# Kernel tuning notes

Measured on AMD Instinct MI355X. Metric: run time of the kernel, lower is better.

The kernel has to match this reference:

```python
import jax, jax.numpy as jnp
import numpy as np

N_NODES = 1_000_000
N_EDGES = 4_000_000  # knn_k = 4
N_GRAPHS = 1024
HIDDEN = 64
N_FEAT = 4


def setup_inputs() -> dict:
    key = jax.random.key(0)
    k0, k1, k2, k3, k4 = jax.random.split(key, 5)
    x = jax.random.normal(k0, (N_NODES, N_FEAT), dtype=jnp.float32)
    edge_index = jax.random.randint(k1, (2, N_EDGES), 0, N_NODES, dtype=jnp.int64)
    batch = jnp.sort(jax.random.randint(k2, (N_NODES,), 0, N_GRAPHS, dtype=jnp.int64))
    W1 = jax.random.normal(k3, (N_FEAT, HIDDEN), dtype=jnp.float32) * 0.5
    b1 = jnp.zeros((HIDDEN,), dtype=jnp.float32)
    W2 = jax.random.normal(k4, (HIDDEN, 1), dtype=jnp.float32) * 0.1
    b2 = jnp.zeros((1,), dtype=jnp.float32)
    return {"x": x, "W1": W1, "b1": b1, "W2": W2, "b2": b2,
            "edge_index": edge_index, "batch": batch}


def gcn_conv(x, edge_index, W, b):
    # PyG GCNConv: linear transform, add self-loops, sym-normalize, scatter-add.
    n = x.shape[0]
    h = x @ W  # [N, 64]
    loop = jnp.arange(n, dtype=edge_index.dtype)
    row = jnp.concatenate([edge_index[0], loop])  # source j
    col = jnp.concatenate([edge_index[1], loop])  # target i
    deg = jax.ops.segment_sum(jnp.ones_like(col, dtype=h.dtype), col, num_segments=n)
    dis = jnp.where(deg > 0, jax.lax.rsqrt(jnp.maximum(deg, 1.0)), 0.0)
    norm = dis[row] * dis[col]  # [E+N]
    out = jax.ops.segment_sum(h[row] * norm[:, None], col, num_segments=n)
    return out + b


def reference(x, W1, b1, W2, b2, edge_index, batch):
    h = gcn_conv(x, edge_index, W1, b1)          # [N, 64]
    h = jax.nn.elu(h)                            # ELU activation
    pooled = jax.ops.segment_sum(h, batch, num_segments=N_GRAPHS)  # global_add_pool
    return pooled @ W2 + b2                      # [G, 1]
```

## Files before the change

kernel.cpp:

```cpp
#include <hip/hip_runtime.h>

#define N_NODES 1000000
#define N_EDGES 4000000
#define N_GRAPHS 1024
#define HIDDEN 64

#define G1 256
#define T1 512
#define EPB (N_EDGES / G1)
#define NB 256
#define BSHIFT 12
#define BSIZE 4096
#define NBUSED ((N_NODES + BSIZE - 1) / BSIZE)

__global__ __launch_bounds__(T1) void k_hist(const int* __restrict__ col,
                                             int* __restrict__ part,
                                             float* __restrict__ out,
                                             const float* __restrict__ b2) {
    __shared__ int h[NB];
    int t = threadIdx.x, blk = blockIdx.x;
    for (int i = t; i < NB; i += T1) h[i] = 0;
    int gid = blk * T1 + t;
    if (gid < N_GRAPHS) out[gid] = b2[0];
    __syncthreads();
    int e0 = blk * EPB;
    for (int i = t; i < EPB; i += T1) {
        int c = col[e0 + i];
        atomicAdd(&h[c >> BSHIFT], 1);
    }
    __syncthreads();
    for (int i = t; i < NB; i += T1) part[blk * NB + i] = h[i];
}

#define G2GROUPS 4
#define BLKS_PER_G (G1 / G2GROUPS)
__global__ __launch_bounds__(1024) void k_off(int* __restrict__ part,
                                              int* __restrict__ ebase,
                                              int* __restrict__ ecnt) {
    __shared__ int tot[G2GROUPS][NB];
    __shared__ int base[NB];
    __shared__ int sc[NB];
    int t = threadIdx.x;
    int q = t >> 8;
    int b = t & 255;
    int run = 0;
    for (int k = 0; k < BLKS_PER_G; ++k) {
        int blk = q * BLKS_PER_G + k;
        int v = part[blk * NB + b];
        part[blk * NB + b] = run;
        run += v;
    }
    tot[q][b] = run;
    __syncthreads();
    if (q == 0) {
        int t0 = tot[0][b], t1 = tot[1][b], t2 = tot[2][b], t3 = tot[3][b];
        int total = t0 + t1 + t2 + t3;
        ecnt[b] = total;
        tot[0][b] = 0;
        tot[1][b] = t0;
        tot[2][b] = t0 + t1;
        tot[3][b] = t0 + t1 + t2;
        sc[b] = total;
    }
    __syncthreads();
    for (int o = 1; o < NB; o <<= 1) {
        int v = 0;
        if (q == 0 && b >= o) v = sc[b - o];
        __syncthreads();
        if (q == 0) sc[b] += v;
        __syncthreads();
    }
    if (q == 0) {
        base[b] = sc[b] - ecnt[b];
        ebase[b] = base[b];
    }
    __syncthreads();
    for (int k = 0; k < BLKS_PER_G; ++k) {
        int blk = q * BLKS_PER_G + k;
        part[blk * NB + b] += tot[q][b] + base[b];
    }
}

__global__ __launch_bounds__(T1) void k_part(const int* __restrict__ row,
                                             const int* __restrict__ col,
                                             const int* __restrict__ part,
                                             unsigned* __restrict__ epair) {
    __shared__ int cur[NB];
    int t = threadIdx.x, blk = blockIdx.x;
    for (int i = t; i < NB; i += T1) cur[i] = part[blk * NB + i];
    __syncthreads();
    int e0 = blk * EPB;
    for (int i = t; i < EPB; i += T1) {
        int c = col[e0 + i];
        int r = row[e0 + i];
        int b = c >> BSHIFT;
        int pos = atomicAdd(&cur[b], 1);
        epair[pos] = ((unsigned)(c & (BSIZE - 1)) << 20) | (unsigned)r;
    }
}

__global__ __launch_bounds__(256) void k_deg2(const unsigned* __restrict__ epair,
                                              const int* __restrict__ ebase,
                                              const int* __restrict__ ecnt,
                                              const float4* __restrict__ x,
                                              float* __restrict__ dis,
                                              float4* __restrict__ xd) {
    __shared__ int deg[BSIZE];
    int t = threadIdx.x, b = blockIdx.x;
    for (int i = t; i < BSIZE; i += 256) deg[i] = 1;
    __syncthreads();
    int e0 = ebase[b], ne = ecnt[b];
    for (int i = t; i < ne; i += 256) {
        unsigned u = epair[e0 + i];
        atomicAdd(&deg[u >> 20], 1);
    }
    __syncthreads();
    int n0 = b << BSHIFT;
    for (int i = t; i < BSIZE; i += 256) {
        int node = n0 + i;
        if (node < N_NODES) {
            float d = rsqrtf((float)deg[i]);
            dis[node] = d;
            float4 xv = x[node];
            xd[node] = make_float4(xv.x * d, xv.y * d, xv.z * d, xv.w * d);
        }
    }
}

__global__ __launch_bounds__(1024) void k_fin(const unsigned* __restrict__ epair,
                                              const int* __restrict__ ebase,
                                              const int* __restrict__ ecnt,
                                              const float4* __restrict__ xd,
                                              const float* __restrict__ dis,
                                              const int* __restrict__ batch,
                                              const float* __restrict__ W1,
                                              const float* __restrict__ b1,
                                              const float* __restrict__ W2,
                                              float* __restrict__ out) {
    __shared__ float4 s4[BSIZE];
    int t = threadIdx.x, b = blockIdx.x;
    for (int i = t; i < BSIZE; i += 1024) s4[i] = make_float4(0.f, 0.f, 0.f, 0.f);
    __syncthreads();
    int e0 = ebase[b], ne = ecnt[b];
    for (int i = t; i < ne; i += 1024) {
        unsigned u = epair[e0 + i];
        int loc = u >> 20;
        int r = (int)(u & 0xFFFFFu);
        float4 v = xd[r];
        float* sp = (float*)&s4[loc];
        atomicAdd(sp + 0, v.x);
        atomicAdd(sp + 1, v.y);
        atomicAdd(sp + 2, v.z);
        atomicAdd(sp + 3, v.w);
    }
    __syncthreads();
    int n0 = b << BSHIFT;
    #pragma unroll
    for (int k = 0; k < BSIZE / 1024; ++k) {
        int ln = t + k * 1024;
        int node = n0 + ln;
        bool valid = node < N_NODES;
        float acc = 0.f;
        int g = -1;
        if (valid) {
            float4 sv = s4[ln];
            float4 xv = xd[node];
            float d = dis[node];
            float u0 = d * (sv.x + xv.x);
            float u1 = d * (sv.y + xv.y);
            float u2 = d * (sv.z + xv.z);
            float u3 = d * (sv.w + xv.w);
            g = batch[node];
            #pragma unroll
            for (int kk = 0; kk < HIDDEN; ++kk) {
                float tt = fmaf(u0, W1[kk],
                           fmaf(u1, W1[HIDDEN + kk],
                           fmaf(u2, W1[2 * HIDDEN + kk],
                           fmaf(u3, W1[3 * HIDDEN + kk], b1[kk]))));
                float h = tt > 0.f ? tt : expm1f(tt);
                acc = fmaf(h, W2[kk], acc);
            }
        }
        unsigned long long rem = __ballot(valid);
        while (rem) {
            int leader = __ffsll(rem) - 1;
            int gl = __shfl(g, leader);
            bool mine = valid && (g == gl);
            unsigned long long mask = __ballot(mine);
            float v = mine ? acc : 0.f;
            #pragma unroll
            for (int o = 32; o; o >>= 1) v += __shfl_xor(v, o);
            if ((int)(t & 63) == leader) unsafeAtomicAdd(&out[gl], v);
            rem &= ~mask;
        }
    }
}

__global__ __launch_bounds__(256) void k_init(int* __restrict__ deg, float4* __restrict__ s,
                                              float* __restrict__ out, const float* __restrict__ b2) {
    int i = blockIdx.x * blockDim.x + threadIdx.x;
    if (i < N_NODES) { deg[i] = 1; s[i] = make_float4(0.f, 0.f, 0.f, 0.f); }
    if (i < N_GRAPHS) out[i] = b2[0];
}
__global__ __launch_bounds__(256) void k_deg(const int* __restrict__ col, int* __restrict__ deg) {
    int e = blockIdx.x * blockDim.x + threadIdx.x;
    if (e < N_EDGES) atomicAdd(&deg[col[e]], 1);
}
__global__ __launch_bounds__(256) void k_dis(const int* __restrict__ deg, float* __restrict__ dis) {
    int i = blockIdx.x * blockDim.x + threadIdx.x;
    if (i < N_NODES) dis[i] = rsqrtf((float)deg[i]);
}
__global__ __launch_bounds__(256) void k_scatter(const int* __restrict__ row, const int* __restrict__ col,
                                                 const float4* __restrict__ x, const float* __restrict__ dis,
                                                 float* __restrict__ s) {
    int e = blockIdx.x * blockDim.x + threadIdx.x;
    if (e >= N_EDGES) return;
    int j = row[e], i = col[e];
    float dj = dis[j];
    float4 xj = x[j];
    float* sp = s + 4ll * (long long)i;
    unsafeAtomicAdd(sp + 0, xj.x * dj);
    unsafeAtomicAdd(sp + 1, xj.y * dj);
    unsafeAtomicAdd(sp + 2, xj.z * dj);
    unsafeAtomicAdd(sp + 3, xj.w * dj);
}
__global__ __launch_bounds__(256) void k_node(const float4* __restrict__ x, const float4* __restrict__ s,
                                              const float* __restrict__ dis, const int* __restrict__ batch,
                                              const float* __restrict__ W1, const float* __restrict__ b1,
                                              const float* __restrict__ W2, float* __restrict__ out) {
    int n = blockIdx.x * blockDim.x + threadIdx.x;
    bool valid = n < N_NODES;
    float acc = 0.f; int g = -1;
    if (valid) {
        float4 xn = x[n], sn = s[n];
        float di = dis[n], inv = di * di;
        float u0 = di * sn.x + inv * xn.x, u1 = di * sn.y + inv * xn.y;
        float u2 = di * sn.z + inv * xn.z, u3 = di * sn.w + inv * xn.w;
        g = batch[n];
        #pragma unroll
        for (int k = 0; k < HIDDEN; ++k) {
            float t = fmaf(u0, W1[k], fmaf(u1, W1[HIDDEN + k],
                      fmaf(u2, W1[2 * HIDDEN + k], fmaf(u3, W1[3 * HIDDEN + k], b1[k]))));
            float h = t > 0.f ? t : expm1f(t);
            acc = fmaf(h, W2[k], acc);
        }
    }
    unsigned long long rem = __ballot(valid);
    while (rem) {
        int leader = __ffsll(rem) - 1;
        int gl = __shfl(g, leader);
        bool mine = valid && (g == gl);
        unsigned long long mask = __ballot(mine);
        float v = mine ? acc : 0.f;
        #pragma unroll
        for (int o = 32; o; o >>= 1) v += __shfl_xor(v, o);
        if ((int)(threadIdx.x & 63) == leader) unsafeAtomicAdd(&out[gl], v);
        rem &= ~mask;
    }
}

extern "C" void kernel_launch(void* const* d_in, const int* in_sizes, int n_in,
                              void* d_out, int out_size, void* d_ws, size_t ws_size,
                              hipStream_t stream) {
    const float* x   = (const float*)d_in[0];
    const float* W1  = (const float*)d_in[1];
    const float* b1  = (const float*)d_in[2];
    const float* W2  = (const float*)d_in[3];
    const float* b2  = (const float*)d_in[4];
    const int*   ei  = (const int*)d_in[5];
    const int*   bat = (const int*)d_in[6];
    float* out = (float*)d_out;

    const int* row = ei;
    const int* col = ei + N_EDGES;
    char* ws = (char*)d_ws;

    size_t o_xd   = 0;
    size_t o_ep   = o_xd + 16000000;
    size_t o_dis  = o_ep + 16000000;
    size_t o_part = o_dis + 4000000;
    size_t o_eb   = o_part + (size_t)G1 * NB * 4;
    size_t o_ec   = o_eb + NB * 4;
    size_t need   = o_ec + NB * 4;

    if (ws_size >= need) {
        float4*   xd    = (float4*)(ws + o_xd);
        unsigned* epair = (unsigned*)(ws + o_ep);
        float*    dis   = (float*)(ws + o_dis);
        int*      part  = (int*)(ws + o_part);
        int*      ebase = (int*)(ws + o_eb);
        int*      ecnt  = (int*)(ws + o_ec);

        k_hist<<<G1, T1, 0, stream>>>(col, part, out, b2);
        k_off<<<1, 1024, 0, stream>>>(part, ebase, ecnt);
        k_part<<<G1, T1, 0, stream>>>(row, col, part, epair);
        k_deg2<<<NBUSED, 256, 0, stream>>>(epair, ebase, ecnt, (const float4*)x, dis, xd);
        k_fin<<<NBUSED, 1024, 0, stream>>>(epair, ebase, ecnt, xd, dis, bat, W1, b1, W2, out);
    } else {
        int nb_n = (N_NODES + 255) / 256;
        int nb_e = (N_EDGES + 255) / 256;
        int*    deg = (int*)(ws);
        float*  dis = (float*)(ws + (size_t)N_NODES * 4);
        float*  s   = (float*)(ws + (size_t)N_NODES * 8);
        float4* s4  = (float4*)s;
        k_init<<<nb_n, 256, 0, stream>>>(deg, s4, out, b2);
        k_deg<<<nb_e, 256, 0, stream>>>(col, deg);
        k_dis<<<nb_n, 256, 0, stream>>>(deg, dis);
        k_scatter<<<nb_e, 256, 0, stream>>>(row, col, (const float4*)x, dis, s);
        k_node<<<nb_n, 256, 0, stream>>>((const float4*)x, s4, dis, bat, W1, b1, W2, out);
    }
}
```

Measured before the change: 210.6 us.

## Store scaled features in fp16, halve buckets, split accumulate and MLP kernels

```diff
diff --git a/kernel.cpp b/kernel.cpp
--- a/kernel.cpp
+++ b/kernel.cpp
@@ -1,4 +1,5 @@
 #include <hip/hip_runtime.h>
+#include <hip/hip_fp16.h>
 
 #define N_NODES 1000000
 #define N_EDGES 4000000
@@ -8,18 +9,18 @@
 #define G1 256
 #define T1 512
 #define EPB (N_EDGES / G1)
-#define NB 256
-#define BSHIFT 12
-#define BSIZE 4096
-#define NBUSED ((N_NODES + BSIZE - 1) / BSIZE)
+#define BSHIFT 11
+#define BSIZE 2048
+#define NBK 512
+#define NBUCK ((N_NODES + BSIZE - 1) / BSIZE)
 
 __global__ __launch_bounds__(T1) void k_hist(const int* __restrict__ col,
                                              int* __restrict__ part,
                                              float* __restrict__ out,
                                              const float* __restrict__ b2) {
-    __shared__ int h[NB];
+    __shared__ int h[NBK];
     int t = threadIdx.x, blk = blockIdx.x;
-    for (int i = t; i < NB; i += T1) h[i] = 0;
+    for (int i = t; i < NBK; i += T1) h[i] = 0;
     int gid = blk * T1 + t;
     if (gid < N_GRAPHS) out[gid] = b2[0];
     __syncthreads();
@@ -29,43 +30,37 @@
         atomicAdd(&h[c >> BSHIFT], 1);
     }
     __syncthreads();
-    for (int i = t; i < NB; i += T1) part[blk * NB + i] = h[i];
-}
-
-#define G2GROUPS 4
-#define BLKS_PER_G (G1 / G2GROUPS)
+    for (int i = t; i < NBK; i += T1) part[blk * NBK + i] = h[i];
+}
+
 __global__ __launch_bounds__(1024) void k_off(int* __restrict__ part,
                                               int* __restrict__ ebase,
                                               int* __restrict__ ecnt) {
-    __shared__ int tot[G2GROUPS][NB];
-    __shared__ int base[NB];
-    __shared__ int sc[NB];
+    __shared__ int tot[2][NBK];
+    __shared__ int sc[NBK];
+    __shared__ int base[NBK];
     int t = threadIdx.x;
-    int q = t >> 8;
-    int b = t & 255;
+    int q = t >> 9;
+    int b = t & (NBK - 1);
     int run = 0;
-    for (int k = 0; k < BLKS_PER_G; ++k) {
-        int blk = q * BLKS_PER_G + k;
-        int v = part[blk * NB + b];
-        part[blk * NB + b] = run;
+    for (int k = 0; k < G1 / 2; ++k) {
+        int blk = q * (G1 / 2) + k;
+        int v = part[blk * NBK + b];
+        part[blk * NBK + b] = run;
         run += v;
     }
     tot[q][b] = run;
     __syncthreads();
     if (q == 0) {
-        int t0 = tot[0][b], t1 = tot[1][b], t2 = tot[2][b], t3 = tot[3][b];
-        int total = t0 + t1 + t2 + t3;
-        ecnt[b] = total;
+        int t0 = tot[0][b], t1 = tot[1][b];
+        ecnt[b] = t0 + t1;
         tot[0][b] = 0;
         tot[1][b] = t0;
-        tot[2][b] = t0 + t1;
-        tot[3][b] = t0 + t1 + t2;
-        sc[b] = total;
-    }
-    __syncthreads();
-    for (int o = 1; o < NB; o <<= 1) {
-        int v = 0;
-        if (q == 0 && b >= o) v = sc[b - o];
+        sc[b] = t0 + t1;
+    }
+    __syncthreads();
+    for (int o = 1; o < NBK; o <<= 1) {
+        int v = (q == 0 && b >= o) ? sc[b - o] : 0;
         __syncthreads();
         if (q == 0) sc[b] += v;
         __syncthreads();
@@ -75,9 +70,10 @@
         ebase[b] = base[b];
     }
     __syncthreads();
-    for (int k = 0; k < BLKS_PER_G; ++k) {
-        int blk = q * BLKS_PER_G + k;
-        part[blk * NB + b] += tot[q][b] + base[b];
+    int add = tot[q][b] + base[b];
+    for (int k = 0; k < G1 / 2; ++k) {
+        int blk = q * (G1 / 2) + k;
+        part[blk * NBK + b] += add;
     }
 }
 
@@ -85,9 +81,9 @@
                                              const int* __restrict__ col,
                                              const int* __restrict__ part,
                                              unsigned* __restrict__ epair) {
-    __shared__ int cur[NB];
+    __shared__ int cur[NBK];
     int t = threadIdx.x, blk = blockIdx.x;
-    for (int i = t; i < NB; i += T1) cur[i] = part[blk * NB + i];
+    for (int i = t; i < NBK; i += T1) cur[i] = part[blk * NBK + i];
     __syncthreads();
     int e0 = blk * EPB;
     for (int i = t; i < EPB; i += T1) {
@@ -104,7 +100,7 @@
                                               const int* __restrict__ ecnt,
                                               const float4* __restrict__ x,
                                               float* __restrict__ dis,
-                                              float4* __restrict__ xd) {
+                                              uint2* __restrict__ xdh) {
     __shared__ int deg[BSIZE];
     int t = threadIdx.x, b = blockIdx.x;
     for (int i = t; i < BSIZE; i += 256) deg[i] = 1;
@@ -122,77 +118,113 @@
             float d = rsqrtf((float)deg[i]);
             dis[node] = d;
             float4 xv = x[node];
-            xd[node] = make_float4(xv.x * d, xv.y * d, xv.z * d, xv.w * d);
+            __half2 h01 = __floats2half2_rn(xv.x * d, xv.y * d);
+            __half2 h23 = __floats2half2_rn(xv.z * d, xv.w * d);
+            uint2 pk;
+            pk.x = *(unsigned*)&h01;
+            pk.y = *(unsigned*)&h23;
+            xdh[node] = pk;
         }
     }
 }
 
-__global__ __launch_bounds__(1024) void k_fin(const unsigned* __restrict__ epair,
+__device__ __forceinline__ void acc_edge(unsigned u, uint2 p, float* sf) {
+    int loc = u >> 20;
+    __half2 h01 = *(__half2*)&p.x;
+    __half2 h23 = *(__half2*)&p.y;
+    float2 f01 = __half22float2(h01);
+    float2 f23 = __half22float2(h23);
+    float* sp = sf + loc * 5;
+    atomicAdd(sp + 0, f01.x);
+    atomicAdd(sp + 1, f01.y);
+    atomicAdd(sp + 2, f23.x);
+    atomicAdd(sp + 3, f23.y);
+}
+
+__global__ __launch_bounds__(1024) void k_acc(const unsigned* __restrict__ epair,
                                               const int* __restrict__ ebase,
                                               const int* __restrict__ ecnt,
-                                              const float4* __restrict__ xd,
-                                              const float* __restrict__ dis,
-                                              const int* __restrict__ batch,
-                                              const float* __restrict__ W1,
-                                              const float* __restrict__ b1,
-                                              const float* __restrict__ W2,
-                                              float* __restrict__ out) {
-    __shared__ float4 s4[BSIZE];
+                                              const uint2* __restrict__ xdh,
+                                              float4* __restrict__ sbuf) {
+    __shared__ float sf[BSIZE * 5];
     int t = threadIdx.x, b = blockIdx.x;
-    for (int i = t; i < BSIZE; i += 1024) s4[i] = make_float4(0.f, 0.f, 0.f, 0.f);
+    for (int i = t; i < BSIZE * 5; i += 1024) sf[i] = 0.f;
     __syncthreads();
     int e0 = ebase[b], ne = ecnt[b];
-    for (int i = t; i < ne; i += 1024) {
-        unsigned u = epair[e0 + i];
-        int loc = u >> 20;
-        int r = (int)(u & 0xFFFFFu);
-        float4 v = xd[r];
-        float* sp = (float*)&s4[loc];
-        atomicAdd(sp + 0, v.x);
-        atomicAdd(sp + 1, v.y);
-        atomicAdd(sp + 2, v.z);
-        atomicAdd(sp + 3, v.w);
+    int ne4 = ne & ~3;
+    const unsigned* ep = epair + e0;
+    for (int i = 4 * t; i < ne4; i += 4096) {
+        unsigned u0 = ep[i], u1 = ep[i + 1], u2 = ep[i + 2], u3 = ep[i + 3];
+        uint2 p0 = xdh[u0 & 0xFFFFFu];
+        uint2 p1 = xdh[u1 & 0xFFFFFu];
+        uint2 p2 = xdh[u2 & 0xFFFFFu];
+        uint2 p3 = xdh[u3 & 0xFFFFFu];
+        acc_edge(u0, p0, sf);
+        acc_edge(u1, p1, sf);
+        acc_edge(u2, p2, sf);
+        acc_edge(u3, p3, sf);
+    }
+    for (int i = ne4 + t; i < ne; i += 1024) {
+        unsigned u = ep[i];
+        acc_edge(u, xdh[u & 0xFFFFFu], sf);
     }
     __syncthreads();
     int n0 = b << BSHIFT;
-    #pragma unroll
-    for (int k = 0; k < BSIZE / 1024; ++k) {
-        int ln = t + k * 1024;
-        int node = n0 + ln;
-        bool valid = node < N_NODES;
-        float acc = 0.f;
-        int g = -1;
-        if (valid) {
-            float4 sv = s4[ln];
-            float4 xv = xd[node];
-            float d = dis[node];
-            float u0 = d * (sv.x + xv.x);
-            float u1 = d * (sv.y + xv.y);
-            float u2 = d * (sv.z + xv.z);
-            float u3 = d * (sv.w + xv.w);
-            g = batch[node];
-            #pragma unroll
-            for (int kk = 0; kk < HIDDEN; ++kk) {
-                float tt = fmaf(u0, W1[kk],
-                           fmaf(u1, W1[HIDDEN + kk],
-                           fmaf(u2, W1[2 * HIDDEN + kk],
-                           fmaf(u3, W1[3 * HIDDEN + kk], b1[kk]))));
-                float h = tt > 0.f ? tt : expm1f(tt);
-                acc = fmaf(h, W2[kk], acc);
-            }
+    for (int i = t; i < BSIZE; i += 1024) {
+        int node = n0 + i;
+        if (node < N_NODES) {
+            const float* sp = sf + i * 5;
+            sbuf[node] = make_float4(sp[0], sp[1], sp[2], sp[3]);
         }
-        unsigned long long rem = __ballot(valid);
-        while (rem) {
-            int leader = __ffsll(rem) - 1;
-            int gl = __shfl(g, leader);
-            bool mine = valid && (g == gl);
-            unsigned long long mask = __ballot(mine);
-            float v = mine ? acc : 0.f;
-            #pragma unroll
-            for (int o = 32; o; o >>= 1) v += __shfl_xor(v, o);
-            if ((int)(t & 63) == leader) unsafeAtomicAdd(&out[gl], v);
-            rem &= ~mask;
+    }
+}
+
+__global__ __launch_bounds__(256) void k_mlp(const float4* __restrict__ sbuf,
+                                             const uint2* __restrict__ xdh,
+                                             const float* __restrict__ dis,
+                                             const int* __restrict__ batch,
+                                             const float* __restrict__ W1,
+                                             const float* __restrict__ b1,
+                                             const float* __restrict__ W2,
+                                             float* __restrict__ out) {
+    int n = blockIdx.x * blockDim.x + threadIdx.x;
+    bool valid = n < N_NODES;
+    float acc = 0.f;
+    int g = -1;
+    if (valid) {
+        float4 sv = sbuf[n];
+        uint2 p = xdh[n];
+        __half2 h01 = *(__half2*)&p.x;
+        __half2 h23 = *(__half2*)&p.y;
+        float2 f01 = __half22float2(h01);
+        float2 f23 = __half22float2(h23);
+        float d = dis[n];
+        float u0 = d * (sv.x + f01.x);
+        float u1 = d * (sv.y + f01.y);
+        float u2 = d * (sv.z + f23.x);
+        float u3 = d * (sv.w + f23.y);
+        g = batch[n];
+        #pragma unroll
+        for (int k = 0; k < HIDDEN; ++k) {
+            float t = fmaf(u0, W1[k],
+                      fmaf(u1, W1[HIDDEN + k],
+                      fmaf(u2, W1[2 * HIDDEN + k],
+                      fmaf(u3, W1[3 * HIDDEN + k], b1[k]))));
+            float h = t > 0.f ? t : (__expf(t) - 1.f);
+            acc = fmaf(h, W2[k], acc);
         }
+    }
+    unsigned long long rem = __ballot(valid);
+    while (rem) {
+        int leader = __ffsll(rem) - 1;
+        int gl = __shfl(g, leader);
+        bool mine = valid && (g == gl);
+        unsigned long long mask = __ballot(mine);
+        float v = mine ? acc : 0.f;
+        #pragma unroll
+        for (int o = 32; o; o >>= 1) v += __shfl_xor(v, o);
+        if ((int)(threadIdx.x & 63) == leader) unsafeAtomicAdd(&out[gl], v);
+        rem &= ~mask;
     }
 }
 
@@ -275,17 +307,19 @@
     const int* col = ei + N_EDGES;
     char* ws = (char*)d_ws;
 
-    size_t o_xd   = 0;
-    size_t o_ep   = o_xd + 16000000;
-    size_t o_dis  = o_ep + 16000000;
+    size_t o_ep   = 0;
+    size_t o_sb   = o_ep + 16000000;
+    size_t o_xdh  = o_sb + 16000000;
+    size_t o_dis  = o_xdh + 8000000;
     size_t o_part = o_dis + 4000000;
-    size_t o_eb   = o_part + (size_t)G1 * NB * 4;
-    size_t o_ec   = o_eb + NB * 4;
-    size_t need   = o_ec + NB * 4;
+    size_t o_eb   = o_part + (size_t)G1 * NBK * 4;
+    size_t o_ec   = o_eb + NBK * 4;
+    size_t need   = o_ec + NBK * 4;
 
     if (ws_size >= need) {
-        float4*   xd    = (float4*)(ws + o_xd);
         unsigned* epair = (unsigned*)(ws + o_ep);
+        float4*   sbuf  = (float4*)(ws + o_sb);
+        uint2*    xdh   = (uint2*)(ws + o_xdh);
         float*    dis   = (float*)(ws + o_dis);
         int*      part  = (int*)(ws + o_part);
         int*      ebase = (int*)(ws + o_eb);
@@ -294,8 +328,9 @@
         k_hist<<<G1, T1, 0, stream>>>(col, part, out, b2);
         k_off<<<1, 1024, 0, stream>>>(part, ebase, ecnt);
         k_part<<<G1, T1, 0, stream>>>(row, col, part, epair);
-        k_deg2<<<NBUSED, 256, 0, stream>>>(epair, ebase, ecnt, (const float4*)x, dis, xd);
-        k_fin<<<NBUSED, 1024, 0, stream>>>(epair, ebase, ecnt, xd, dis, bat, W1, b1, W2, out);
+        k_deg2<<<NBUCK, 256, 0, stream>>>(epair, ebase, ecnt, (const float4*)x, dis, xdh);
+        k_acc<<<NBUCK, 1024, 0, stream>>>(epair, ebase, ecnt, xdh, sbuf);
+        k_mlp<<<(N_NODES + 255) / 256, 256, 0, stream>>>(sbuf, xdh, dis, bat, W1, b1, W2, out);
     } else {
         int nb_n = (N_NODES + 255) / 256;
         int nb_e = (N_EDGES + 255) / 256;
```

New measurement: 198.9 us. 5.5% less time.
